# Performance work log

Measured on AMD Instinct MI355X. Metric: run time of the kernel, lower is better.

## Reference

```python
import jax, jax.numpy as jnp
import numpy as np

N, E, NC, ES, NT, G = 200000, 500000, 150000, 350000, 100000, 1024
FN, FE, H, T = 133, 14, 128, 3


def _enc_params(key, prefix):
    ks = jax.random.split(key, 4)
    g = lambda k, shape, fan_in: jax.random.normal(k, shape, jnp.float32) / np.sqrt(fan_in).astype(np.float32)
    return {
        f"{prefix}_w_node": g(ks[0], (FN, H), FN),
        f"{prefix}_b_node": jnp.zeros((H,), jnp.float32),
        f"{prefix}_w_edge": g(ks[1], (FE, H), FE),
        f"{prefix}_b_edge": jnp.zeros((H,), jnp.float32),
        f"{prefix}_w_mp": g(ks[2], (T, H, H), H),
        f"{prefix}_b_mp": jnp.zeros((T, H), jnp.float32),
        f"{prefix}_w_out": g(ks[3], (H, H), H),
        f"{prefix}_b_out": jnp.zeros((H,), jnp.float32),
    }


def setup_inputs() -> dict:
    key = jax.random.key(0)
    k = lambda i: jax.random.fold_in(key, i)
    inp = {
        "x": jax.random.normal(k(0), (N, FN), jnp.float32),
        "node_weight": jax.random.uniform(k(1), (N,), jnp.float32),
        "edge_index": jax.random.randint(k(2), (2, E), 0, N),
        "edge_attr": jax.random.normal(k(3), (E, FE), jnp.float32),
        "edge_weight": jax.random.uniform(k(4), (E,), jnp.float32),
        "batch": jnp.sort(jax.random.randint(k(5), (N,), 0, G)),
        "context_nodes_mapper": jax.random.randint(k(6), (NC,), 0, N),
        "target_nodes_mapper": jax.random.randint(k(7), (NT,), 0, N),
        "combined_subgraphs": jax.random.randint(k(8), (2, ES), 0, NC),
        "subgraphs_edges_mapper": jax.random.randint(k(9), (ES,), 0, E),
        "context_edges_mask": jax.random.bernoulli(k(10), 0.7, (ES,)),
    }
    inp.update(_enc_params(k(11), "ctx"))
    inp.update(_enc_params(k(12), "tgt"))
    return inp


def wd_mpnn(x, src, dst, edge_attr, edge_weight, node_weight,
            w_node, b_node, w_edge, b_edge, w_mp, b_mp, w_out, b_out, n_nodes):
    # Weighted-edge node MPNN: gather source node states, combine with edge
    # embedding, scale by edge weight, scatter-sum onto destination nodes.
    h = jax.nn.relu(x @ w_node + b_node)                 # [n_nodes, H]
    eh = jax.nn.relu(edge_attr @ w_edge + b_edge)        # [n_edges, H]
    ew = edge_weight[:, None]
    for t in range(w_mp.shape[0]):
        msg = ew * (h[src] + eh)                         # gather [n_edges, H]
        agg = jax.ops.segment_sum(msg, dst, num_segments=n_nodes)
        h = jax.nn.relu(h + agg @ w_mp[t] + b_mp[t])
    return (h @ w_out + b_out) * node_weight[:, None]


def segment_mean(vals, seg, num_segments):
    s = jax.ops.segment_sum(vals, seg, num_segments=num_segments)
    c = jax.ops.segment_sum(jnp.ones((vals.shape[0],), vals.dtype), seg, num_segments=num_segments)
    return s / jnp.maximum(c, 1.0)[:, None]


def reference(x, node_weight, edge_index, edge_attr, edge_weight, batch,
              context_nodes_mapper, target_nodes_mapper, combined_subgraphs,
              subgraphs_edges_mapper, context_edges_mask,
              ctx_w_node, ctx_b_node, ctx_w_edge, ctx_b_edge, ctx_w_mp, ctx_b_mp, ctx_w_out, ctx_b_out,
              tgt_w_node, tgt_b_node, tgt_w_edge, tgt_b_edge, tgt_w_mp, tgt_b_mp, tgt_w_out, tgt_b_out):
    # --- context branch: gather subgraph node/edge features ---
    cx = x[context_nodes_mapper]                         # [NC, FN]
    cnw = node_weight[context_nodes_mapper]              # [NC]
    cea = edge_attr[subgraphs_edges_mapper]              # [ES, FE]
    # boolean edge mask folded into edge weights (messages scale linearly in
    # edge_weight, so zeroing masked edges == dropping them) -> jit friendly
    cew = edge_weight[subgraphs_edges_mapper] * context_edges_mask.astype(jnp.float32)
    csrc, cdst = combined_subgraphs[0], combined_subgraphs[1]
    ctx_nodes = wd_mpnn(cx, csrc, cdst, cea, cew, cnw,
                        ctx_w_node, ctx_b_node, ctx_w_edge, ctx_b_edge,
                        ctx_w_mp, ctx_b_mp, ctx_w_out, ctx_b_out, NC)
    ctx_emb = segment_mean(ctx_nodes, batch[context_nodes_mapper], G)   # [G, H]

    # --- target branch: full-graph encode, pool over target nodes ---
    full = wd_mpnn(x, edge_index[0], edge_index[1], edge_attr, edge_weight, node_weight,
                   tgt_w_node, tgt_b_node, tgt_w_edge, tgt_b_edge,
                   tgt_w_mp, tgt_b_mp, tgt_w_out, tgt_b_out, N)
    tgt_emb = segment_mean(full[target_nodes_mapper], batch[target_nodes_mapper], G)  # [G, H]

    return jnp.stack([ctx_emb, tgt_emb])                 # [2, G, H]
```

## Files before the change

### kernel.cpp

```cpp
#include <hip/hip_runtime.h>
#include <stdint.h>

#define H 128
#define FN 133
#define FE 14
#define NG 1024
#define APAD 132

__global__ void k_sniff(const unsigned int* __restrict__ w, int nwords, int* __restrict__ flag) {
    __shared__ int sawFloat, sawBig;
    if (threadIdx.x == 0) { sawFloat = 0; sawBig = 0; }
    __syncthreads();
    int f = 0, bg = 0;
    for (int i = threadIdx.x; i < nwords; i += blockDim.x) {
        unsigned int v = w[i];
        if (v == 0u || v == 1u) continue;
        if (v == 0x3F800000u) f = 1; else bg = 1;
    }
    if (f) atomicOr(&sawFloat, 1);
    if (bg) atomicOr(&sawBig, 1);
    __syncthreads();
    if (threadIdx.x == 0) *flag = sawBig ? 1 : (sawFloat ? 2 : 0);
}

__device__ __forceinline__ float mask_val(const void* mask, int mm, long e) {
    if (mm == 1)      return ((const unsigned char*)mask)[e] ? 1.f : 0.f;
    else if (mm == 2) return ((const float*)mask)[e];
    else              return ((const int*)mask)[e] ? 1.f : 0.f;
}

template<bool GATHER>
__global__ __launch_bounds__(256)
void k_gemm_enc(const float* __restrict__ x, const int* __restrict__ map, int nrows,
                const float* __restrict__ w, const float* __restrict__ bias,
                float* __restrict__ hout) {
    __shared__ float w_lds[32][H];
    __shared__ float a_lds[32][APAD];
    __shared__ int   m_lds[128];
    const int tid = threadIdx.x;
    const int rbase = blockIdx.x * 128;
    if (GATHER && tid < 128) {
        int row = rbase + tid;
        m_lds[tid] = (row < nrows) ? map[row] : 0;
    }
    const int tx = tid & 15, ty = tid >> 4;
    float acc[8][8] = {};
    for (int kc = 0; kc < 5; ++kc) {
        const int k0 = kc * 32;
        __syncthreads();
        for (int i = tid; i < 32 * 32; i += 256) {
            int kk = i >> 5, c4 = i & 31;
            float4 v = make_float4(0.f, 0.f, 0.f, 0.f);
            if (k0 + kk < FN)
                v = reinterpret_cast<const float4*>(w + (size_t)(k0 + kk) * H)[c4];
            *reinterpret_cast<float4*>(&w_lds[kk][c4 * 4]) = v;
        }
        for (int i = tid; i < 128 * 32; i += 256) {
            int r = i >> 5, kk = i & 31;
            int row = rbase + r;
            float v = 0.f;
            if (row < nrows && k0 + kk < FN) {
                int sr = GATHER ? m_lds[r] : row;
                v = x[(size_t)sr * FN + k0 + kk];
            }
            a_lds[kk][r] = v;
        }
        __syncthreads();
        #pragma unroll 4
        for (int k = 0; k < 32; ++k) {
            float4 a0 = *reinterpret_cast<const float4*>(&a_lds[k][ty * 8]);
            float4 a1 = *reinterpret_cast<const float4*>(&a_lds[k][ty * 8 + 4]);
            float4 w0 = *reinterpret_cast<const float4*>(&w_lds[k][tx * 8]);
            float4 w1 = *reinterpret_cast<const float4*>(&w_lds[k][tx * 8 + 4]);
            float aa[8] = {a0.x, a0.y, a0.z, a0.w, a1.x, a1.y, a1.z, a1.w};
            float ww[8] = {w0.x, w0.y, w0.z, w0.w, w1.x, w1.y, w1.z, w1.w};
            #pragma unroll
            for (int i2 = 0; i2 < 8; ++i2)
                #pragma unroll
                for (int j = 0; j < 8; ++j)
                    acc[i2][j] += aa[i2] * ww[j];
        }
    }
    float4 b0 = reinterpret_cast<const float4*>(bias)[tx * 2];
    float4 b1 = reinterpret_cast<const float4*>(bias)[tx * 2 + 1];
    float bb[8] = {b0.x, b0.y, b0.z, b0.w, b1.x, b1.y, b1.z, b1.w};
    #pragma unroll
    for (int i2 = 0; i2 < 8; ++i2) {
        int row = rbase + ty * 8 + i2;
        if (row < nrows) {
            float4 o0, o1;
            o0.x = fmaxf(acc[i2][0] + bb[0], 0.f); o0.y = fmaxf(acc[i2][1] + bb[1], 0.f);
            o0.z = fmaxf(acc[i2][2] + bb[2], 0.f); o0.w = fmaxf(acc[i2][3] + bb[3], 0.f);
            o1.x = fmaxf(acc[i2][4] + bb[4], 0.f); o1.y = fmaxf(acc[i2][5] + bb[5], 0.f);
            o1.z = fmaxf(acc[i2][6] + bb[6], 0.f); o1.w = fmaxf(acc[i2][7] + bb[7], 0.f);
            float* hp = hout + (size_t)row * H + tx * 8;
            *reinterpret_cast<float4*>(hp)     = o0;
            *reinterpret_cast<float4*>(hp + 4) = o1;
        }
    }
}

template<int MODE>
__global__ __launch_bounds__(256)
void k_hist(const int* __restrict__ dst, const float* __restrict__ edge_weight,
            const int* __restrict__ emap, const void* __restrict__ mask,
            const int* __restrict__ mmode_p, int* __restrict__ deg, int nedges) {
    int e = blockIdx.x * 256 + threadIdx.x;
    if (e >= nedges) return;
    int eo = MODE ? emap[e] : e;
    float w = edge_weight[eo];
    if (MODE) w *= mask_val(mask, *mmode_p, e);
    if (w != 0.f) atomicAdd(&deg[dst[e]], 1);
}

__global__ __launch_bounds__(256)
void k_scan1(const int* __restrict__ deg, int* __restrict__ off, int* __restrict__ bsum, int n) {
    __shared__ int tsum[256];
    const int tid = threadIdx.x;
    const int base = blockIdx.x * 1024;
    int local[4]; int s = 0;
    #pragma unroll
    for (int j = 0; j < 4; ++j) {
        int i = base + tid * 4 + j;
        local[j] = (i < n) ? deg[i] : 0;
        s += local[j];
    }
    tsum[tid] = s;
    __syncthreads();
    for (int d = 1; d < 256; d <<= 1) {
        int v = (tid >= d) ? tsum[tid - d] : 0;
        __syncthreads();
        tsum[tid] += v;
        __syncthreads();
    }
    int excl = tsum[tid] - s;
    #pragma unroll
    for (int j = 0; j < 4; ++j) {
        int i = base + tid * 4 + j;
        if (i < n) off[i] = excl;
        excl += local[j];
    }
    if (tid == 255) bsum[blockIdx.x] = tsum[255];
}

__global__ __launch_bounds__(256)
void k_scan2(int* __restrict__ bsum, int nb) {
    __shared__ int tsum[256];
    const int tid = threadIdx.x;
    int local[4]; int s = 0;
    #pragma unroll
    for (int j = 0; j < 4; ++j) {
        int i = tid * 4 + j;
        local[j] = (i < nb) ? bsum[i] : 0;
        s += local[j];
    }
    tsum[tid] = s;
    __syncthreads();
    for (int d = 1; d < 256; d <<= 1) {
        int v = (tid >= d) ? tsum[tid - d] : 0;
        __syncthreads();
        tsum[tid] += v;
        __syncthreads();
    }
    int excl = tsum[tid] - s;
    #pragma unroll
    for (int j = 0; j < 4; ++j) {
        int i = tid * 4 + j;
        if (i < nb) bsum[i] = excl;
        excl += local[j];
    }
}

__global__ __launch_bounds__(256)
void k_scan3(const int* __restrict__ bsum, int* __restrict__ off, int* __restrict__ cur, int n) {
    int i = blockIdx.x * 256 + threadIdx.x;
    if (i < n) {
        int o = off[i] + bsum[i >> 10];
        off[i] = o;
        cur[i] = o;
    }
}

template<int MODE>
__global__ __launch_bounds__(256)
void k_scatter(const int* __restrict__ src, const int* __restrict__ dst,
               const float* __restrict__ edge_weight,
               const int* __restrict__ emap, const void* __restrict__ mask,
               const int* __restrict__ mmode_p, int* __restrict__ cur,
               int* __restrict__ esrc, float* __restrict__ eew, int* __restrict__ eeo,
               int nedges) {
    int e = blockIdx.x * 256 + threadIdx.x;
    if (e >= nedges) return;
    int eo = MODE ? emap[e] : e;
    float w = edge_weight[eo];
    if (MODE) w *= mask_val(mask, *mmode_p, e);
    if (w != 0.f) {
        int pos = atomicAdd(&cur[dst[e]], 1);
        esrc[pos] = src[e];
        eew[pos]  = w;
        eeo[pos]  = eo;
    }
}

__global__ __launch_bounds__(256)
void k_eh_csr(const int* __restrict__ off, const int* __restrict__ deg,
              const float* __restrict__ eew, const int* __restrict__ eeo,
              const float* __restrict__ edge_attr,
              const float* __restrict__ w_edge, const float* __restrict__ b_edge,
              float* __restrict__ aggeh, int nnodes) {
    __shared__ float we_lds[FE * H];
    __shared__ float be_lds[H];
    for (int i = threadIdx.x; i < FE * H; i += 256) we_lds[i] = w_edge[i];
    if (threadIdx.x < H) be_lds[threadIdx.x] = b_edge[threadIdx.x];
    __syncthreads();
    const int hw = threadIdx.x >> 5;
    const int ln = threadIdx.x & 31;
    const int c  = ln * 4;
    int v = blockIdx.x * 8 + hw;
    if (v >= nnodes) return;
    float4 acc = make_float4(0.f, 0.f, 0.f, 0.f);
    const int o = off[v], d = deg[v];
    const float4 bev = *reinterpret_cast<const float4*>(be_lds + c);
    for (int j = o; j < o + d; ++j) {
        float w = eew[j];
        int eo  = eeo[j];
        const float* ea = edge_attr + (size_t)eo * FE;
        float myea = (ln < FE) ? ea[ln] : 0.f;
        float4 eh = bev;
        #pragma unroll
        for (int k = 0; k < FE; ++k) {
            float a = __shfl(myea, k, 32);
            const float* wr = we_lds + k * H + c;
            eh.x += a * wr[0]; eh.y += a * wr[1]; eh.z += a * wr[2]; eh.w += a * wr[3];
        }
        acc.x += w * fmaxf(eh.x, 0.f); acc.y += w * fmaxf(eh.y, 0.f);
        acc.z += w * fmaxf(eh.z, 0.f); acc.w += w * fmaxf(eh.w, 0.f);
    }
    *reinterpret_cast<float4*>(aggeh + (size_t)v * H + c) = acc;
}

__global__ __launch_bounds__(256)
void k_msg_csr(const int* __restrict__ off, const int* __restrict__ deg,
               const int* __restrict__ esrc, const float* __restrict__ eew,
               const float* __restrict__ h, float* __restrict__ agg, int nnodes) {
    const int hw = threadIdx.x >> 5;
    const int c  = (threadIdx.x & 31) * 4;
    int v = blockIdx.x * 8 + hw;
    if (v >= nnodes) return;
    float4 acc = make_float4(0.f, 0.f, 0.f, 0.f);
    const int o = off[v], d = deg[v];
    int j = o, e = o + d;
    for (; j + 2 <= e; j += 2) {
        int   s0 = esrc[j],   s1 = esrc[j + 1];
        float w0 = eew[j],    w1 = eew[j + 1];
        float4 v0 = *reinterpret_cast<const float4*>(h + (size_t)s0 * H + c);
        float4 v1 = *reinterpret_cast<const float4*>(h + (size_t)s1 * H + c);
        acc.x += w0 * v0.x; acc.y += w0 * v0.y; acc.z += w0 * v0.z; acc.w += w0 * v0.w;
        acc.x += w1 * v1.x; acc.y += w1 * v1.y; acc.z += w1 * v1.z; acc.w += w1 * v1.w;
    }
    if (j < e) {
        float w0 = eew[j];
        float4 v0 = *reinterpret_cast<const float4*>(h + (size_t)esrc[j] * H + c);
        acc.x += w0 * v0.x; acc.y += w0 * v0.y; acc.z += w0 * v0.z; acc.w += w0 * v0.w;
    }
    *reinterpret_cast<float4*>(agg + (size_t)v * H + c) = acc;
}

__global__ __launch_bounds__(256)
void k_gemm_update(const float* __restrict__ agg, const float* __restrict__ aggeh, int nrows,
                   const float* __restrict__ w, const float* __restrict__ bias,
                   float* __restrict__ h) {
    __shared__ float w_lds[32][H];
    __shared__ float a_lds[32][APAD];
    const int tid = threadIdx.x;
    const int rbase = blockIdx.x * 128;
    const int tx = tid & 15, ty = tid >> 4;
    float acc[8][8] = {};
    for (int kc = 0; kc < 4; ++kc) {
        const int k0 = kc * 32;
        __syncthreads();
        for (int i = tid; i < 1024; i += 256) {
            int kk = i >> 5, c4 = i & 31;
            *reinterpret_cast<float4*>(&w_lds[kk][c4 * 4]) =
                reinterpret_cast<const float4*>(w + (size_t)(k0 + kk) * H)[c4];
        }
        for (int i = tid; i < 1024; i += 256) {
            int r = i >> 3, f = i & 7;
            int row = rbase + r;
            float4 v = make_float4(0.f, 0.f, 0.f, 0.f);
            if (row < nrows) {
                size_t base = (size_t)row * H + k0;
                float4 va = reinterpret_cast<const float4*>(agg + base)[f];
                float4 vb = reinterpret_cast<const float4*>(aggeh + base)[f];
                v.x = va.x + vb.x; v.y = va.y + vb.y; v.z = va.z + vb.z; v.w = va.w + vb.w;
            }
            a_lds[f * 4 + 0][r] = v.x;
            a_lds[f * 4 + 1][r] = v.y;
            a_lds[f * 4 + 2][r] = v.z;
            a_lds[f * 4 + 3][r] = v.w;
        }
        __syncthreads();
        #pragma unroll 4
        for (int k = 0; k < 32; ++k) {
            float4 a0 = *reinterpret_cast<const float4*>(&a_lds[k][ty * 8]);
            float4 a1 = *reinterpret_cast<const float4*>(&a_lds[k][ty * 8 + 4]);
            float4 w0 = *reinterpret_cast<const float4*>(&w_lds[k][tx * 8]);
            float4 w1 = *reinterpret_cast<const float4*>(&w_lds[k][tx * 8 + 4]);
            float aa[8] = {a0.x, a0.y, a0.z, a0.w, a1.x, a1.y, a1.z, a1.w};
            float ww[8] = {w0.x, w0.y, w0.z, w0.w, w1.x, w1.y, w1.z, w1.w};
            #pragma unroll
            for (int i2 = 0; i2 < 8; ++i2)
                #pragma unroll
                for (int j = 0; j < 8; ++j)
                    acc[i2][j] += aa[i2] * ww[j];
        }
    }
    float4 b0 = reinterpret_cast<const float4*>(bias)[tx * 2];
    float4 b1 = reinterpret_cast<const float4*>(bias)[tx * 2 + 1];
    float bb[8] = {b0.x, b0.y, b0.z, b0.w, b1.x, b1.y, b1.z, b1.w};
    #pragma unroll
    for (int i2 = 0; i2 < 8; ++i2) {
        int row = rbase + ty * 8 + i2;
        if (row < nrows) {
            float* hp = h + (size_t)row * H + tx * 8;
            float4 h0 = *reinterpret_cast<const float4*>(hp);
            float4 h1 = *reinterpret_cast<const float4*>(hp + 4);
            float4 o0, o1;
            o0.x = fmaxf(h0.x + acc[i2][0] + bb[0], 0.f); o0.y = fmaxf(h0.y + acc[i2][1] + bb[1], 0.f);
            o0.z = fmaxf(h0.z + acc[i2][2] + bb[2], 0.f); o0.w = fmaxf(h0.w + acc[i2][3] + bb[3], 0.f);
            o1.x = fmaxf(h1.x + acc[i2][4] + bb[4], 0.f); o1.y = fmaxf(h1.y + acc[i2][5] + bb[5], 0.f);
            o1.z = fmaxf(h1.z + acc[i2][6] + bb[6], 0.f); o1.w = fmaxf(h1.w + acc[i2][7] + bb[7], 0.f);
            *reinterpret_cast<float4*>(hp)     = o0;
            *reinterpret_cast<float4*>(hp + 4) = o1;
        }
    }
}

__global__ __launch_bounds__(256)
void k_ghist(const int* __restrict__ rowmap, const int* __restrict__ batch,
             int* __restrict__ deg_g, int nrows) {
    int r = blockIdx.x * 256 + threadIdx.x;
    if (r < nrows) atomicAdd(&deg_g[batch[rowmap[r]]], 1);
}

__global__ __launch_bounds__(256)
void k_gscan(const int* __restrict__ deg, int* __restrict__ off, int* __restrict__ cur) {
    __shared__ int tsum[256];
    const int tid = threadIdx.x;
    int local[4]; int s = 0;
    #pragma unroll
    for (int j = 0; j < 4; ++j) { local[j] = deg[tid * 4 + j]; s += local[j]; }
    tsum[tid] = s;
    __syncthreads();
    for (int d = 1; d < 256; d <<= 1) {
        int v = (tid >= d) ? tsum[tid - d] : 0;
        __syncthreads();
        tsum[tid] += v;
        __syncthreads();
    }
    int excl = tsum[tid] - s;
    #pragma unroll
    for (int j = 0; j < 4; ++j) {
        off[tid * 4 + j] = excl;
        cur[tid * 4 + j] = excl;
        excl += local[j];
    }
}

template<bool GATHER>
__global__ __launch_bounds__(256)
void k_gscatter(const int* __restrict__ rowmap, const int* __restrict__ batch,
                const float* __restrict__ nodew, int* __restrict__ cur,
                int* __restrict__ prow, float* __restrict__ pnw, int nrows) {
    int r = blockIdx.x * 256 + threadIdx.x;
    if (r >= nrows) return;
    int oid = rowmap[r];
    int g = batch[oid];
    int pos = atomicAdd(&cur[g], 1);
    prow[pos] = GATHER ? oid : r;
    pnw[pos]  = nodew[oid];
}

__global__ __launch_bounds__(256)
void k_pool(const int* __restrict__ off_g, const int* __restrict__ deg_g,
            const int* __restrict__ prow, const float* __restrict__ pnw,
            const float* __restrict__ h,
            const float* __restrict__ w, const float* __restrict__ bias,
            float* __restrict__ outp) {
    __shared__ float s_lds[4][H];
    __shared__ float ssum[H];
    __shared__ float r_lds[2][H];
    __shared__ float cg_lds[4];
    const int g = blockIdx.x;
    const int o = off_g[g], cnt = deg_g[g];
    const int wv = threadIdx.x >> 6, lane = threadIdx.x & 63;
    float ax = 0.f, ay = 0.f, cg = 0.f;
    for (int i = wv; i < cnt; i += 4) {
        int hrow = prow[o + i];
        float nw = pnw[o + i];
        float2 v = *reinterpret_cast<const float2*>(h + (size_t)hrow * H + lane * 2);
        ax += nw * v.x; ay += nw * v.y; cg += nw;
    }
    s_lds[wv][lane * 2]     = ax;
    s_lds[wv][lane * 2 + 1] = ay;
    if (lane == 0) cg_lds[wv] = cg;
    __syncthreads();
    if (threadIdx.x < H)
        ssum[threadIdx.x] = s_lds[0][threadIdx.x] + s_lds[1][threadIdx.x]
                          + s_lds[2][threadIdx.x] + s_lds[3][threadIdx.x];
    __syncthreads();
    const int c = threadIdx.x & 127, kh = threadIdx.x >> 7;
    float p = 0.f;
    #pragma unroll 8
    for (int k = 0; k < 64; ++k)
        p += ssum[kh * 64 + k] * w[(size_t)(kh * 64 + k) * H + c];
    r_lds[kh][c] = p;
    __syncthreads();
    if (threadIdx.x < H) {
        float cga = cg_lds[0] + cg_lds[1] + cg_lds[2] + cg_lds[3];
        float val = r_lds[0][c] + r_lds[1][c] + bias[c] * cga;
        outp[(size_t)g * H + c] = val / fmaxf((float)cnt, 1.f);
    }
}

extern "C" void kernel_launch(void* const* d_in, const int* in_sizes, int n_in,
                              void* d_out, int out_size, void* d_ws, size_t ws_size,
                              hipStream_t stream) {
    (void)n_in; (void)out_size; (void)ws_size;
    const float* x           = (const float*)d_in[0];
    const float* node_weight = (const float*)d_in[1];
    const int*   edge_index  = (const int*)d_in[2];
    const float* edge_attr   = (const float*)d_in[3];
    const float* edge_weight = (const float*)d_in[4];
    const int*   batch       = (const int*)d_in[5];
    const int*   cnm         = (const int*)d_in[6];
    const int*   tnm         = (const int*)d_in[7];
    const int*   csub        = (const int*)d_in[8];
    const int*   sem         = (const int*)d_in[9];
    const void*  cmask       = d_in[10];

    const float* ctx_w_node = (const float*)d_in[11];
    const float* ctx_b_node = (const float*)d_in[12];
    const float* ctx_w_edge = (const float*)d_in[13];
    const float* ctx_b_edge = (const float*)d_in[14];
    const float* ctx_w_mp   = (const float*)d_in[15];
    const float* ctx_b_mp   = (const float*)d_in[16];
    const float* ctx_w_out  = (const float*)d_in[17];
    const float* ctx_b_out  = (const float*)d_in[18];
    const float* tgt_w_node = (const float*)d_in[19];
    const float* tgt_b_node = (const float*)d_in[20];
    const float* tgt_w_edge = (const float*)d_in[21];
    const float* tgt_b_edge = (const float*)d_in[22];
    const float* tgt_w_mp   = (const float*)d_in[23];
    const float* tgt_b_mp   = (const float*)d_in[24];
    const float* tgt_w_out  = (const float*)d_in[25];
    const float* tgt_b_out  = (const float*)d_in[26];

    const int N  = in_sizes[1];
    const int E  = in_sizes[4];
    const int NC = in_sizes[6];
    const int NT = in_sizes[7];
    const int ES = in_sizes[9];
    const int NMAX = (NT > NC) ? NT : NC;

    float* out = (float*)d_out;

    char* ws = (char*)d_ws;
    float* h      = (float*)ws;  ws += (size_t)N * H * sizeof(float);
    float* agg    = (float*)ws;  ws += (size_t)N * H * sizeof(float);
    float* aggeh  = (float*)ws;  ws += (size_t)N * H * sizeof(float);
    int*   deg    = (int*)ws;    ws += (size_t)N * sizeof(int);
    int*   off    = (int*)ws;    ws += (size_t)N * sizeof(int);
    int*   cur    = (int*)ws;    ws += (size_t)N * sizeof(int);
    int*   bsum   = (int*)ws;    ws += 1024 * sizeof(int);
    int*   esrc   = (int*)ws;    ws += (size_t)E * sizeof(int);
    float* eew    = (float*)ws;  ws += (size_t)E * sizeof(float);
    int*   eeo    = (int*)ws;    ws += (size_t)E * sizeof(int);
    int*   deg_g  = (int*)ws;    ws += NG * sizeof(int);
    int*   off_g  = (int*)ws;    ws += NG * sizeof(int);
    int*   cur_g  = (int*)ws;    ws += NG * sizeof(int);
    int*   prow   = (int*)ws;    ws += (size_t)NMAX * sizeof(int);
    float* pnw    = (float*)ws;  ws += (size_t)NMAX * sizeof(float);
    int*   flag   = (int*)ws;    ws += sizeof(int);

    int nwords = ES / 4; if (nwords > 8192) nwords = 8192;
    k_sniff<<<1, 256, 0, stream>>>((const unsigned int*)cmask, nwords, flag);

    {
        const int* fsrc = edge_index;
        const int* fdst = edge_index + E;
        hipMemsetAsync(deg, 0, (size_t)N * sizeof(int), stream);
        int egrid = (E + 255) / 256;
        k_hist<0><<<egrid, 256, 0, stream>>>(fdst, edge_weight, nullptr, nullptr, nullptr, deg, E);
        int nb1 = (N + 1023) / 1024;
        k_scan1<<<nb1, 256, 0, stream>>>(deg, off, bsum, N);
        k_scan2<<<1, 256, 0, stream>>>(bsum, nb1);
        k_scan3<<<(N + 255) / 256, 256, 0, stream>>>(bsum, off, cur, N);
        k_scatter<0><<<egrid, 256, 0, stream>>>(fsrc, fdst, edge_weight, nullptr, nullptr, nullptr,
                                                cur, esrc, eew, eeo, E);
        k_gemm_enc<false><<<(N + 127) / 128, 256, 0, stream>>>(x, nullptr, N, tgt_w_node, tgt_b_node, h);
        k_eh_csr<<<(N + 7) / 8, 256, 0, stream>>>(off, deg, eew, eeo, edge_attr,
                                                  tgt_w_edge, tgt_b_edge, aggeh, N);
        for (int t = 0; t < 3; ++t) {
            k_msg_csr<<<(N + 7) / 8, 256, 0, stream>>>(off, deg, esrc, eew, h, agg, N);
            k_gemm_update<<<(N + 127) / 128, 256, 0, stream>>>(agg, aggeh, N,
                                                               tgt_w_mp + t * H * H, tgt_b_mp + t * H, h);
        }
        hipMemsetAsync(deg_g, 0, NG * sizeof(int), stream);
        k_ghist<<<(NT + 255) / 256, 256, 0, stream>>>(tnm, batch, deg_g, NT);
        k_gscan<<<1, 256, 0, stream>>>(deg_g, off_g, cur_g);
        k_gscatter<true><<<(NT + 255) / 256, 256, 0, stream>>>(tnm, batch, node_weight, cur_g, prow, pnw, NT);
        k_pool<<<NG, 256, 0, stream>>>(off_g, deg_g, prow, pnw, h, tgt_w_out, tgt_b_out,
                                       out + (size_t)NG * H);
    }

    {
        const int* csrc = csub;
        const int* cdst = csub + ES;
        hipMemsetAsync(deg, 0, (size_t)NC * sizeof(int), stream);
        int egrid = (ES + 255) / 256;
        k_hist<1><<<egrid, 256, 0, stream>>>(cdst, edge_weight, sem, cmask, flag, deg, ES);
        int nb1 = (NC + 1023) / 1024;
        k_scan1<<<nb1, 256, 0, stream>>>(deg, off, bsum, NC);
        k_scan2<<<1, 256, 0, stream>>>(bsum, nb1);
        k_scan3<<<(NC + 255) / 256, 256, 0, stream>>>(bsum, off, cur, NC);
        k_scatter<1><<<egrid, 256, 0, stream>>>(csrc, cdst, edge_weight, sem, cmask, flag,
                                                cur, esrc, eew, eeo, ES);
        k_gemm_enc<true><<<(NC + 127) / 128, 256, 0, stream>>>(x, cnm, NC, ctx_w_node, ctx_b_node, h);
        k_eh_csr<<<(NC + 7) / 8, 256, 0, stream>>>(off, deg, eew, eeo, edge_attr,
                                                   ctx_w_edge, ctx_b_edge, aggeh, NC);
        for (int t = 0; t < 3; ++t) {
            k_msg_csr<<<(NC + 7) / 8, 256, 0, stream>>>(off, deg, esrc, eew, h, agg, NC);
            k_gemm_update<<<(NC + 127) / 128, 256, 0, stream>>>(agg, aggeh, NC,
                                                                ctx_w_mp + t * H * H, ctx_b_mp + t * H, h);
        }
        hipMemsetAsync(deg_g, 0, NG * sizeof(int), stream);
        k_ghist<<<(NC + 255) / 256, 256, 0, stream>>>(cnm, batch, deg_g, NC);
        k_gscan<<<1, 256, 0, stream>>>(deg_g, off_g, cur_g);
        k_gscatter<false><<<(NC + 255) / 256, 256, 0, stream>>>(cnm, batch, node_weight, cur_g, prow, pnw, NC);
        k_pool<<<NG, 256, 0, stream>>>(off_g, deg_g, prow, pnw, h, ctx_w_out, ctx_b_out, out);
    }
}
```

Before: 1.766 ms.

## Pack CSR edge metadata into int2 and warp-broadcast it in gather kernels

The scatter step now writes (src, weight) and (edge_id, weight) as packed int2 arrays instead of three separate int/float arrays. The message and edge-embedding kernels load up to 32 edges' metadata with one coalesced load per lane and broadcast each entry via shuffles, which removes the dependent scalar loads per edge. The message kernel also unrolls by 4 (2 for the edge kernel) to keep more gathers in flight. It starts its accumulator from aggeh, so the GEMM-update no longer reads a second N×H buffer. In exchange the weight is stored twice, and padded unroll slots issue dummy loads of row 0.

```diff
diff --git a/kernel.cpp b/kernel.cpp
--- a/kernel.cpp
+++ b/kernel.cpp
@@ -187,7 +187,7 @@
                const float* __restrict__ edge_weight,
                const int* __restrict__ emap, const void* __restrict__ mask,
                const int* __restrict__ mmode_p, int* __restrict__ cur,
-               int* __restrict__ esrc, float* __restrict__ eew, int* __restrict__ eeo,
+               int2* __restrict__ epk, int2* __restrict__ epkh,
                int nedges) {
     int e = blockIdx.x * 256 + threadIdx.x;
     if (e >= nedges) return;
@@ -196,15 +196,15 @@
     if (MODE) w *= mask_val(mask, *mmode_p, e);
     if (w != 0.f) {
         int pos = atomicAdd(&cur[dst[e]], 1);
-        esrc[pos] = src[e];
-        eew[pos]  = w;
-        eeo[pos]  = eo;
+        int wb = __float_as_int(w);
+        epk[pos]  = make_int2(src[e], wb);
+        epkh[pos] = make_int2(eo, wb);
     }
 }
 
 __global__ __launch_bounds__(256)
 void k_eh_csr(const int* __restrict__ off, const int* __restrict__ deg,
-              const float* __restrict__ eew, const int* __restrict__ eeo,
+              const int2* __restrict__ epkh,
               const float* __restrict__ edge_attr,
               const float* __restrict__ w_edge, const float* __restrict__ b_edge,
               float* __restrict__ aggeh, int nnodes) {
@@ -221,53 +221,74 @@
     float4 acc = make_float4(0.f, 0.f, 0.f, 0.f);
     const int o = off[v], d = deg[v];
     const float4 bev = *reinterpret_cast<const float4*>(be_lds + c);
-    for (int j = o; j < o + d; ++j) {
-        float w = eew[j];
-        int eo  = eeo[j];
-        const float* ea = edge_attr + (size_t)eo * FE;
-        float myea = (ln < FE) ? ea[ln] : 0.f;
-        float4 eh = bev;
-        #pragma unroll
-        for (int k = 0; k < FE; ++k) {
-            float a = __shfl(myea, k, 32);
-            const float* wr = we_lds + k * H + c;
-            eh.x += a * wr[0]; eh.y += a * wr[1]; eh.z += a * wr[2]; eh.w += a * wr[3];
-        }
-        acc.x += w * fmaxf(eh.x, 0.f); acc.y += w * fmaxf(eh.y, 0.f);
-        acc.z += w * fmaxf(eh.z, 0.f); acc.w += w * fmaxf(eh.w, 0.f);
+    for (int jb = 0; jb < d; jb += 32) {
+        const int nn = min(32, d - jb);
+        int2 meta = make_int2(0, 0);
+        if (ln < nn) meta = epkh[o + jb + ln];
+        const int me = meta.x;
+        const float mw = __int_as_float(meta.y);
+        for (int q = 0; q < nn; q += 2) {
+            int   e0 = __shfl(me, q, 32);
+            float w0 = __shfl(mw, q, 32);
+            int   e1 = __shfl(me, q + 1, 32);
+            float w1 = __shfl(mw, q + 1, 32);
+            bool ok1 = (q + 1 < nn);
+            if (!ok1) { e1 = e0; w1 = 0.f; }
+            float a0 = (ln < FE) ? edge_attr[(size_t)e0 * FE + ln] : 0.f;
+            float a1 = (ln < FE) ? edge_attr[(size_t)e1 * FE + ln] : 0.f;
+            float4 eh0 = bev, eh1 = bev;
+            #pragma unroll
+            for (int k = 0; k < FE; ++k) {
+                float f0 = __shfl(a0, k, 32);
+                float f1 = __shfl(a1, k, 32);
+                float4 wv = *reinterpret_cast<const float4*>(we_lds + k * H + c);
+                eh0.x += f0 * wv.x; eh0.y += f0 * wv.y; eh0.z += f0 * wv.z; eh0.w += f0 * wv.w;
+                eh1.x += f1 * wv.x; eh1.y += f1 * wv.y; eh1.z += f1 * wv.z; eh1.w += f1 * wv.w;
+            }
+            acc.x += w0 * fmaxf(eh0.x, 0.f) + w1 * fmaxf(eh1.x, 0.f);
+            acc.y += w0 * fmaxf(eh0.y, 0.f) + w1 * fmaxf(eh1.y, 0.f);
+            acc.z += w0 * fmaxf(eh0.z, 0.f) + w1 * fmaxf(eh1.z, 0.f);
+            acc.w += w0 * fmaxf(eh0.w, 0.f) + w1 * fmaxf(eh1.w, 0.f);
+        }
     }
     *reinterpret_cast<float4*>(aggeh + (size_t)v * H + c) = acc;
 }
 
 __global__ __launch_bounds__(256)
 void k_msg_csr(const int* __restrict__ off, const int* __restrict__ deg,
-               const int* __restrict__ esrc, const float* __restrict__ eew,
+               const int2* __restrict__ epk, const float* __restrict__ aggeh,
                const float* __restrict__ h, float* __restrict__ agg, int nnodes) {
     const int hw = threadIdx.x >> 5;
     const int c  = (threadIdx.x & 31) * 4;
+    const int ln = threadIdx.x & 31;
     int v = blockIdx.x * 8 + hw;
     if (v >= nnodes) return;
-    float4 acc = make_float4(0.f, 0.f, 0.f, 0.f);
+    float4 acc = *reinterpret_cast<const float4*>(aggeh + (size_t)v * H + c);
     const int o = off[v], d = deg[v];
-    int j = o, e = o + d;
-    for (; j + 2 <= e; j += 2) {
-        int   s0 = esrc[j],   s1 = esrc[j + 1];
-        float w0 = eew[j],    w1 = eew[j + 1];
-        float4 v0 = *reinterpret_cast<const float4*>(h + (size_t)s0 * H + c);
-        float4 v1 = *reinterpret_cast<const float4*>(h + (size_t)s1 * H + c);
-        acc.x += w0 * v0.x; acc.y += w0 * v0.y; acc.z += w0 * v0.z; acc.w += w0 * v0.w;
-        acc.x += w1 * v1.x; acc.y += w1 * v1.y; acc.z += w1 * v1.z; acc.w += w1 * v1.w;
-    }
-    if (j < e) {
-        float w0 = eew[j];
-        float4 v0 = *reinterpret_cast<const float4*>(h + (size_t)esrc[j] * H + c);
-        acc.x += w0 * v0.x; acc.y += w0 * v0.y; acc.z += w0 * v0.z; acc.w += w0 * v0.w;
+    for (int jb = 0; jb < d; jb += 32) {
+        const int nn = min(32, d - jb);
+        int2 meta = make_int2(0, 0);
+        if (ln < nn) meta = epk[o + jb + ln];
+        const int ms = meta.x;
+        const float mw = __int_as_float(meta.y);
+        for (int q = 0; q < nn; q += 4) {
+            #pragma unroll
+            for (int u = 0; u < 4; ++u) {
+                int qq = q + u;
+                int   s = __shfl(ms, qq, 32);
+                float w = __shfl(mw, qq, 32);
+                if (qq >= nn) { s = 0; w = 0.f; }
+                float4 hv = *reinterpret_cast<const float4*>(h + (size_t)s * H + c);
+                acc.x += w * hv.x; acc.y += w * hv.y;
+                acc.z += w * hv.z; acc.w += w * hv.w;
+            }
+        }
     }
     *reinterpret_cast<float4*>(agg + (size_t)v * H + c) = acc;
 }
 
 __global__ __launch_bounds__(256)
-void k_gemm_update(const float* __restrict__ agg, const float* __restrict__ aggeh, int nrows,
+void k_gemm_update(const float* __restrict__ agg, int nrows,
                    const float* __restrict__ w, const float* __restrict__ bias,
                    float* __restrict__ h) {
     __shared__ float w_lds[32][H];
@@ -288,12 +309,8 @@
             int r = i >> 3, f = i & 7;
             int row = rbase + r;
             float4 v = make_float4(0.f, 0.f, 0.f, 0.f);
-            if (row < nrows) {
-                size_t base = (size_t)row * H + k0;
-                float4 va = reinterpret_cast<const float4*>(agg + base)[f];
-                float4 vb = reinterpret_cast<const float4*>(aggeh + base)[f];
-                v.x = va.x + vb.x; v.y = va.y + vb.y; v.z = va.z + vb.z; v.w = va.w + vb.w;
-            }
+            if (row < nrows)
+                v = reinterpret_cast<const float4*>(agg + (size_t)row * H + k0)[f];
             a_lds[f * 4 + 0][r] = v.x;
             a_lds[f * 4 + 1][r] = v.y;
             a_lds[f * 4 + 2][r] = v.z;
@@ -469,13 +486,12 @@
     float* h      = (float*)ws;  ws += (size_t)N * H * sizeof(float);
     float* agg    = (float*)ws;  ws += (size_t)N * H * sizeof(float);
     float* aggeh  = (float*)ws;  ws += (size_t)N * H * sizeof(float);
+    int2*  epk    = (int2*)ws;   ws += (size_t)E * sizeof(int2);
+    int2*  epkh   = (int2*)ws;   ws += (size_t)E * sizeof(int2);
     int*   deg    = (int*)ws;    ws += (size_t)N * sizeof(int);
     int*   off    = (int*)ws;    ws += (size_t)N * sizeof(int);
     int*   cur    = (int*)ws;    ws += (size_t)N * sizeof(int);
     int*   bsum   = (int*)ws;    ws += 1024 * sizeof(int);
-    int*   esrc   = (int*)ws;    ws += (size_t)E * sizeof(int);
-    float* eew    = (float*)ws;  ws += (size_t)E * sizeof(float);
-    int*   eeo    = (int*)ws;    ws += (size_t)E * sizeof(int);
     int*   deg_g  = (int*)ws;    ws += NG * sizeof(int);
     int*   off_g  = (int*)ws;    ws += NG * sizeof(int);
     int*   cur_g  = (int*)ws;    ws += NG * sizeof(int);
@@ -497,13 +513,13 @@
         k_scan2<<<1, 256, 0, stream>>>(bsum, nb1);
         k_scan3<<<(N + 255) / 256, 256, 0, stream>>>(bsum, off, cur, N);
         k_scatter<0><<<egrid, 256, 0, stream>>>(fsrc, fdst, edge_weight, nullptr, nullptr, nullptr,
-                                                cur, esrc, eew, eeo, E);
+                                                cur, epk, epkh, E);
         k_gemm_enc<false><<<(N + 127) / 128, 256, 0, stream>>>(x, nullptr, N, tgt_w_node, tgt_b_node, h);
-        k_eh_csr<<<(N + 7) / 8, 256, 0, stream>>>(off, deg, eew, eeo, edge_attr,
+        k_eh_csr<<<(N + 7) / 8, 256, 0, stream>>>(off, deg, epkh, edge_attr,
                                                   tgt_w_edge, tgt_b_edge, aggeh, N);
         for (int t = 0; t < 3; ++t) {
-            k_msg_csr<<<(N + 7) / 8, 256, 0, stream>>>(off, deg, esrc, eew, h, agg, N);
-            k_gemm_update<<<(N + 127) / 128, 256, 0, stream>>>(agg, aggeh, N,
+            k_msg_csr<<<(N + 7) / 8, 256, 0, stream>>>(off, deg, epk, aggeh, h, agg, N);
+            k_gemm_update<<<(N + 127) / 128, 256, 0, stream>>>(agg, N,
                                                                tgt_w_mp + t * H * H, tgt_b_mp + t * H, h);
         }
         hipMemsetAsync(deg_g, 0, NG * sizeof(int), stream);
@@ -525,13 +541,13 @@
         k_scan2<<<1, 256, 0, stream>>>(bsum, nb1);
         k_scan3<<<(NC + 255) / 256, 256, 0, stream>>>(bsum, off, cur, NC);
         k_scatter<1><<<egrid, 256, 0, stream>>>(csrc, cdst, edge_weight, sem, cmask, flag,
-                                                cur, esrc, eew, eeo, ES);
+                                                cur, epk, epkh, ES);
         k_gemm_enc<true><<<(NC + 127) / 128, 256, 0, stream>>>(x, cnm, NC, ctx_w_node, ctx_b_node, h);
-        k_eh_csr<<<(NC + 7) / 8, 256, 0, stream>>>(off, deg, eew, eeo, edge_attr,
+        k_eh_csr<<<(NC + 7) / 8, 256, 0, stream>>>(off, deg, epkh, edge_attr,
                                                    ctx_w_edge, ctx_b_edge, aggeh, NC);
         for (int t = 0; t < 3; ++t) {
-            k_msg_csr<<<(NC + 7) / 8, 256, 0, stream>>>(off, deg, esrc, eew, h, agg, NC);
-            k_gemm_update<<<(NC + 127) / 128, 256, 0, stream>>>(agg, aggeh, NC,
+            k_msg_csr<<<(NC + 7) / 8, 256, 0, stream>>>(off, deg, epk, aggeh, h, agg, NC);
+            k_gemm_update<<<(NC + 127) / 128, 256, 0, stream>>>(agg, NC,
                                                                 ctx_w_mp + t * H * H, ctx_b_mp + t * H, h);
         }
         hipMemsetAsync(deg_g, 0, NG * sizeof(int), stream);
```

Measured after the change: 1.700 ms. 1.04x faster.
